# Performance work log

Hardware: AMD Instinct MI355X
Metric: run time of the kernel (lower is better)

## Reference

```python
import jax, jax.numpy as jnp
import numpy as np

NUM_HEADS = 16
NUM_KV_HEADS = 8
HEAD_DIM = 128
ROPE_THETA = 10000.0
SOFTCAP = 50.0


def rotate_half(x):
    x1, x2 = jnp.split(x, 2, axis=-1)
    return jnp.concatenate((-x2, x1), axis=-1)


def rope_cos_sin(seq_len):
    inv_freq = 1.0 / (ROPE_THETA ** (jnp.arange(0, HEAD_DIM, 2, dtype=jnp.float32) / HEAD_DIM))
    t = jnp.arange(seq_len, dtype=jnp.float32)
    freqs = t[:, None] * inv_freq[None, :]          # [S, D/2]
    emb = jnp.concatenate((freqs, freqs), axis=-1)  # [S, D]
    return jnp.cos(emb), jnp.sin(emb)


def setup_inputs() -> dict:
    key = jax.random.key(0)
    k1, k2, k3, k4, k5 = jax.random.split(key, 5)
    B, S, H = 2, 2048, 2048
    sc = 1.0 / np.sqrt(H)
    return {
        "hidden_states": jax.random.normal(k1, (B, S, H), dtype=jnp.float32),
        "Wq": jax.random.normal(k2, (H, NUM_HEADS * HEAD_DIM), dtype=jnp.float32) * sc,
        "Wk": jax.random.normal(k3, (H, NUM_KV_HEADS * HEAD_DIM), dtype=jnp.float32) * sc,
        "Wv": jax.random.normal(k4, (H, NUM_KV_HEADS * HEAD_DIM), dtype=jnp.float32) * sc,
        "Wo": jax.random.normal(k5, (NUM_HEADS * HEAD_DIM, H), dtype=jnp.float32) * sc,
    }


def reference(hidden_states, Wq, Wk, Wv, Wo):
    B, S, _ = hidden_states.shape
    groups = NUM_HEADS // NUM_KV_HEADS

    # projections -> [B, heads, S, D]
    q = (hidden_states @ Wq).reshape(B, S, NUM_HEADS, HEAD_DIM).transpose(0, 2, 1, 3)
    k = (hidden_states @ Wk).reshape(B, S, NUM_KV_HEADS, HEAD_DIM).transpose(0, 2, 1, 3)
    v = (hidden_states @ Wv).reshape(B, S, NUM_KV_HEADS, HEAD_DIM).transpose(0, 2, 1, 3)

    cos, sin = rope_cos_sin(S)  # [S, D], broadcast over (B, heads)
    q = q * cos + rotate_half(q) * sin
    k = k * cos + rotate_half(k) * sin

    # GQA: expand KV heads (repeat_interleave along head dim)
    k = jnp.repeat(k, groups, axis=1)
    v = jnp.repeat(v, groups, axis=1)

    scores = jnp.einsum('bhsd,bhtd->bhst', q, k) / np.sqrt(HEAD_DIM)
    scores = jnp.tanh(scores / SOFTCAP) * SOFTCAP  # Gemma logit softcapping
    weights = jax.nn.softmax(scores.astype(jnp.float32), axis=-1).astype(q.dtype)

    out = jnp.einsum('bhst,bhtd->bhsd', weights, v)
    out = out.transpose(0, 2, 1, 3).reshape(B, S, NUM_HEADS * HEAD_DIM)
    return out @ Wo
```

## Files before the change

kernel.cpp:

```cpp
#include <hip/hip_runtime.h>
#include <math.h>

typedef __bf16 bf16;
typedef __bf16 bf16x8 __attribute__((ext_vector_type(8)));
typedef __bf16 bf16x4 __attribute__((ext_vector_type(4)));
typedef float f32x2 __attribute__((ext_vector_type(2)));
typedef float f32x4 __attribute__((ext_vector_type(4)));
typedef float f32x16 __attribute__((ext_vector_type(16)));
typedef unsigned int uint;
typedef uint u32x4 __attribute__((ext_vector_type(4)));
typedef uint u32x2 __attribute__((ext_vector_type(2)));
typedef __bf16 bf16x8_a __attribute__((ext_vector_type(8), __may_alias__));
typedef uint u32x2_a __attribute__((ext_vector_type(2), __may_alias__));
typedef __bf16 bf16x4_a __attribute__((ext_vector_type(4), __may_alias__));
typedef __bf16 bf16_a __attribute__((__may_alias__));

constexpr int BATCH = 2;
constexpr int SEQ   = 2048;
constexpr int HID   = 2048;
constexpr int NHEAD = 16;
constexpr int NKV   = 8;
constexpr int HD    = 128;
constexpr int MROWS = BATCH * SEQ;

#define DEVINL __device__ __forceinline__

#define BAR()                                 \
  do {                                        \
    asm volatile("" ::: "memory");            \
    __builtin_amdgcn_s_barrier();             \
    asm volatile("" ::: "memory");            \
  } while (0)

#define WAITV(N) asm volatile("s_waitcnt vmcnt(" #N ")" ::: "memory")

DEVINL void async16(void* l, const void* g) {
  __builtin_amdgcn_global_load_lds((const __attribute__((address_space(1))) void*)g,
                                   (__attribute__((address_space(3))) void*)l, 16, 0, 0);
}

DEVINL f32x4 mfma16(bf16x8 a, bf16x8 b, f32x4 c) {
  return __builtin_amdgcn_mfma_f32_16x16x32_bf16(a, b, c, 0, 0, 0);
}
DEVINL f32x16 mfma32(bf16x8 a, bf16x8 b, f32x16 c) {
  return __builtin_amdgcn_mfma_f32_32x32x16_bf16(a, b, c, 0, 0, 0);
}

DEVINL f32x4 fzero4() { f32x4 z; z[0] = 0.f; z[1] = 0.f; z[2] = 0.f; z[3] = 0.f; return z; }

DEVINL float ex2(float x) {
#if __has_builtin(__builtin_amdgcn_exp2f)
  return __builtin_amdgcn_exp2f(x);
#else
  return __expf(x * 0.6931471805599453f);
#endif
}

DEVINL uint pkbf16(float lo, float hi) {
  unsigned short l = __builtin_bit_cast(unsigned short, (bf16)lo);
  unsigned short h = __builtin_bit_cast(unsigned short, (bf16)hi);
  return (uint)l | ((uint)h << 16);
}

DEVINL u32x2 pswap(uint a, uint b) {
#if __has_builtin(__builtin_amdgcn_permlane32_swap)
  return __builtin_amdgcn_permlane32_swap(a, b, false, false);
#else
  int hl = (int)((threadIdx.x >> 5) & 1);
  uint as = __shfl_xor(a, 32), bs = __shfl_xor(b, 32);
  u32x2 r;
  r[0] = hl ? bs : a;
  r[1] = hl ? b : as;
  return r;
#endif
}

__global__ __launch_bounds__(256) void prep(const float* __restrict__ X,
                                            const float* __restrict__ Wq,
                                            const float* __restrict__ Wk,
                                            const float* __restrict__ Wv,
                                            const float* __restrict__ Wo,
                                            bf16* __restrict__ Xb,
                                            bf16* __restrict__ WqT, bf16* __restrict__ WkT,
                                            bf16* __restrict__ WvT, bf16* __restrict__ WoT,
                                            float* __restrict__ ct, float* __restrict__ st) {
  const int tid = threadIdx.x;
  const int z = blockIdx.z;
  if (z == 4) {
    int idx = (blockIdx.y * 32 + blockIdx.x) * 256 + tid;
    if (idx < SEQ * 64) {
      int s = idx >> 6, d = idx & 63;
      float freq = powf(10000.0f, -(float)d * (1.0f / 64.0f));
      float a = (float)s * freq;
      ct[idx] = cosf(a);
      st[idx] = sinf(a);
    }
    return;
  }
  if (z == 5) {
    int j = (blockIdx.y * 32 + blockIdx.x) * 256 + tid;
#pragma unroll
    for (int it = 0; it < 8; it++) {
      int e = (it * 262144 + j) * 4;
      float4 v = *(const float4*)(X + e);
      bf16x4 o;
      o[0] = (bf16)v.x; o[1] = (bf16)v.y; o[2] = (bf16)v.z; o[3] = (bf16)v.w;
      *(bf16x4*)(Xb + e) = o;
    }
    return;
  }
  __shared__ bf16 t[64][65];
  const float* W; bf16* WT; int N;
  switch (z) {
    case 0: W = Wq; WT = WqT; N = 2048; break;
    case 1: W = Wk; WT = WkT; N = 1024; break;
    case 2: W = Wv; WT = WvT; N = 1024; break;
    default: W = Wo; WT = WoT; N = 2048; break;
  }
  int n0 = blockIdx.x * 64, k0 = blockIdx.y * 64;
  if (n0 >= N) return;
#pragma unroll
  for (int p = 0; p < 4; p++) {
    int r = (tid >> 4) + p * 16;
    int c4 = (tid & 15) * 4;
    float4 v = *(const float4*)(&W[(size_t)(k0 + r) * N + n0 + c4]);
    t[r][c4 + 0] = (bf16)v.x;
    t[r][c4 + 1] = (bf16)v.y;
    t[r][c4 + 2] = (bf16)v.z;
    t[r][c4 + 3] = (bf16)v.w;
  }
  __syncthreads();
#pragma unroll
  for (int p = 0; p < 4; p++) {
    int nr = (tid >> 4) + p * 16;
    int kb = (tid & 15) * 4;
    bf16x4 o;
    o[0] = t[kb + 0][nr];
    o[1] = t[kb + 1][nr];
    o[2] = t[kb + 2][nr];
    o[3] = t[kb + 3][nr];
    *(bf16x4_a*)(&WT[(size_t)(n0 + nr) * 2048 + k0 + kb]) = o;
  }
}

__global__ __launch_bounds__(256) void vtrans(const bf16* __restrict__ V, bf16* __restrict__ VT) {
  __shared__ bf16 t[64][65];
  int s0 = blockIdx.x * 64, d0 = blockIdx.y * 64;
  int bh = blockIdx.z, b = bh >> 3, kvh = bh & 7;
  for (int i = threadIdx.x; i < 4096; i += 256) {
    int r = i >> 6, c = i & 63;
    t[r][c] = V[(size_t)(b * SEQ + s0 + r) * (NKV * HD) + kvh * HD + d0 + c];
  }
  __syncthreads();
  for (int i = threadIdx.x; i < 4096; i += 256) {
    int r = i >> 6, c = i & 63;
    VT[((size_t)bh * HD + d0 + r) * SEQ + s0 + c] = t[c][r];
  }
}

template <int EPI>
__global__ __launch_bounds__(512, 2) void gemm8p(const bf16* __restrict__ A,
                                                 const bf16* __restrict__ BT,
                                                 void* __restrict__ C0, void* __restrict__ C1,
                                                 void* __restrict__ C2, int M, int N, int K,
                                                 const float* __restrict__ ct,
                                                 const float* __restrict__ st) {
  __shared__ alignas(16) char ldsA[65536];
  __shared__ alignas(16) char ldsB[65536];
  const int tid = threadIdx.x, lane = tid & 63, w = tid >> 6;
  const int l15 = lane & 15, l4 = lane >> 4;
  const int wm = w >> 2, wn = w & 3;
  const int gx = gridDim.x;
  const int nwg = gx * gridDim.y;
  int id = blockIdx.y * gx + blockIdx.x;
  id = (id & 7) * (nwg >> 3) + (id >> 3);
  const int row0 = (id / gx) * 256;
  const int col0 = (id % gx) * 256;

  f32x4 acc[8][4];
#pragma unroll
  for (int mt = 0; mt < 8; mt++)
#pragma unroll
    for (int nt = 0; nt < 4; nt++) acc[mt][nt] = fzero4();

  const int rG0 = tid >> 3, sG0 = ((tid & 7) ^ (rG0 & 7)) * 8;
  const int ci1 = 512 + tid;
  const int rG1 = ci1 >> 3, sG1 = ((ci1 & 7) ^ (rG1 & 7)) * 8;
  const int dst0 = tid * 16, dst1 = (512 + tid) * 16;

  const bf16* Asrc = A + (size_t)row0 * K;
  const bf16* Bsrc = BT + (size_t)col0 * K;
  const int nk = K >> 6;

#define STG_A(half, kt, buf)                                         \
  {                                                                  \
    char* d = ldsA + (buf) * 32768 + (half) * 16384;                 \
    const bf16* s = Asrc + (size_t)((half) * 128) * K + (kt) * 64;   \
    async16(d + dst0, s + (size_t)rG0 * K + sG0);                    \
    async16(d + dst1, s + (size_t)rG1 * K + sG1);                    \
  }
#define STG_B(half, kt, buf)                                         \
  {                                                                  \
    char* d = ldsB + (buf) * 32768 + (half) * 16384;                 \
    const bf16* s = Bsrc + (size_t)((half) * 128) * K + (kt) * 64;   \
    async16(d + dst0, s + (size_t)rG0 * K + sG0);                    \
    async16(d + dst1, s + (size_t)rG1 * K + sG1);                    \
  }

  STG_A(0, 0, 0) STG_A(1, 0, 0) STG_B(0, 0, 0) STG_B(1, 0, 0)
  STG_B(0, 1, 1) STG_B(1, 1, 1) STG_A(0, 1, 1) STG_A(1, 1, 1)
  WAITV(8);
  BAR();

  bf16x8 af[8];
  bf16x8 bfr[2][4];

  for (int t = 0; t < nk; ++t) {
    const int buf = t & 1;
    const char* bA = ldsA + buf * 32768 + wm * 16384;
    const char* bB = ldsB + buf * 32768;
    const bool s2 = (t + 2) < nk;

#pragma unroll
    for (int mtp = 0; mtp < 4; mtp++)
#pragma unroll
      for (int kc = 0; kc < 2; kc++) {
        int r = mtp * 16 + l15;
        int off = ((r << 7) + ((kc * 4 + l4) << 4)) ^ ((r & 7) << 4);
        af[mtp * 2 + kc] = *(const bf16x8_a*)(bA + off);
      }
#pragma unroll
    for (int ntp = 0; ntp < 2; ntp++)
#pragma unroll
      for (int kc = 0; kc < 2; kc++) {
        int c = wn * 16 + ntp * 64 + l15;
        int off = ((c << 7) + ((kc * 4 + l4) << 4)) ^ ((c & 7) << 4);
        bfr[0][ntp * 2 + kc] = *(const bf16x8_a*)(bB + off);
        bfr[1][ntp * 2 + kc] = *(const bf16x8_a*)(bB + 16384 + off);
      }
    BAR();
    if (s2) { STG_B(0, t + 2, buf) STG_B(1, t + 2, buf) }
    __builtin_amdgcn_s_setprio(1);
#pragma unroll
    for (int mtp = 0; mtp < 4; mtp++)
#pragma unroll
      for (int half = 0; half < 2; half++)
#pragma unroll
        for (int ntp = 0; ntp < 2; ntp++)
#pragma unroll
          for (int kc = 0; kc < 2; kc++)
            acc[mtp][half * 2 + ntp] =
                mfma16(af[mtp * 2 + kc], bfr[half][ntp * 2 + kc], acc[mtp][half * 2 + ntp]);
    __builtin_amdgcn_s_setprio(0);
    BAR();

#pragma unroll
    for (int mtp = 0; mtp < 4; mtp++)
#pragma unroll
      for (int kc = 0; kc < 2; kc++) {
        int r = 64 + mtp * 16 + l15;
        int off = ((r << 7) + ((kc * 4 + l4) << 4)) ^ ((r & 7) << 4);
        af[mtp * 2 + kc] = *(const bf16x8_a*)(bA + off);
      }
    BAR();
    if (s2) { STG_A(0, t + 2, buf) STG_A(1, t + 2, buf) }
    __builtin_amdgcn_s_setprio(1);
#pragma unroll
    for (int mtp = 0; mtp < 4; mtp++)
#pragma unroll
      for (int half = 0; half < 2; half++)
#pragma unroll
        for (int ntp = 0; ntp < 2; ntp++)
#pragma unroll
          for (int kc = 0; kc < 2; kc++)
            acc[mtp + 4][half * 2 + ntp] =
                mfma16(af[mtp * 2 + kc], bfr[half][ntp * 2 + kc], acc[mtp + 4][half * 2 + ntp]);
    __builtin_amdgcn_s_setprio(0);
    if (s2) { WAITV(8); } else { WAITV(0); }
    BAR();
  }
#undef STG_A
#undef STG_B

#pragma unroll
  for (int mt = 0; mt < 8; mt++)
#pragma unroll
    for (int nt = 0; nt < 4; nt++)
#pragma unroll
      for (int rg = 0; rg < 4; rg++) {
        int row = row0 + wm * 128 + mt * 16 + l4 * 4 + rg;
        int ntL = (nt & 1) + (nt >> 1) * 2;
        int cl = col0 + wn * 16 + ((nt >> 1) * 128) + ((nt & 1) * 64);
        (void)ntL;
        float v = acc[mt][nt][rg];
        cl += l15;
        if (EPI == 2) {
          ((float*)C0)[(size_t)row * N + cl] = v;
        } else {
          if (cl < 3072) {
            int s = row & (SEQ - 1);
            float cc = ct[s * 64 + wn * 16 + l15];
            float ss = st[s * 64 + wn * 16 + l15];
            float pv = acc[mt][nt ^ 1][rg];
            v = (nt & 1) ? fmaf(v, cc, pv * ss) : fmaf(v, cc, -pv * ss);
          }
          if (cl < 2048) {
            v *= 1.7677669529663689e-3f;
            ((bf16*)C0)[(size_t)row * 2048 + cl] = (bf16)v;
          } else if (cl < 3072) {
            ((bf16*)C1)[(size_t)row * 1024 + (cl - 2048)] = (bf16)v;
          } else {
            ((bf16*)C2)[(size_t)row * 1024 + (cl - 3072)] = (bf16)v;
          }
        }
      }
}

__global__ __launch_bounds__(512, 2) void gemm2p(const bf16* __restrict__ A,
                                                 const bf16* __restrict__ BT,
                                                 float* __restrict__ C, int M, int N, int K) {
  __shared__ alignas(16) char ldsA[65536];
  __shared__ alignas(16) char ldsB[49152];
  const int tid = threadIdx.x, lane = tid & 63, w = tid >> 6;
  const int l15 = lane & 15, l4 = lane >> 4;
  const int wm = w >> 1, wn = w & 1;
  const int gx = gridDim.x;
  const int nwg = gx * gridDim.y;
  int id = blockIdx.y * gx + blockIdx.x;
  id = (id & 7) * (nwg >> 3) + (id >> 3);
  const int row0 = (id / gx) * 256;
  const int col0 = (id % gx) * 128;

  f32x4 acc[4][4];
#pragma unroll
  for (int mt = 0; mt < 4; mt++)
#pragma unroll
    for (int nt = 0; nt < 4; nt++) acc[mt][nt] = fzero4();

  const int rG0 = tid >> 3, sG0 = ((tid & 7) ^ (rG0 & 7)) * 8;
  const int ci1 = 512 + tid;
  const int rG1 = ci1 >> 3, sG1 = ((ci1 & 7) ^ (rG1 & 7)) * 8;
  const int dst0 = tid * 16, dst1 = (512 + tid) * 16;

  const bf16* Asrc = A + (size_t)row0 * K;
  const bf16* Bsrc = BT + (size_t)col0 * K;
  const int nk = K >> 6;

#define STG_A2(half, kt, buf)                                        \
  {                                                                  \
    char* d = ldsA + (buf) * 32768 + (half) * 16384;                 \
    const bf16* s = Asrc + (size_t)((half) * 128) * K + (kt) * 64;   \
    async16(d + dst0, s + (size_t)rG0 * K + sG0);                    \
    async16(d + dst1, s + (size_t)rG1 * K + sG1);                    \
  }
#define STG_B2(kt, buf)                                              \
  {                                                                  \
    char* d = ldsB + (buf) * 16384;                                  \
    const bf16* s = Bsrc + (kt) * 64;                                \
    async16(d + dst0, s + (size_t)rG0 * K + sG0);                    \
    async16(d + dst1, s + (size_t)rG1 * K + sG1);                    \
  }

  STG_B2(0, 0) STG_A2(0, 0, 0) STG_A2(1, 0, 0)
  STG_B2(1, 1) STG_A2(0, 1, 1) STG_A2(1, 1, 1)
  WAITV(6);
  BAR();

  bf16x8 af[8];
  bf16x8 bfr[8];

  for (int t = 0; t < nk; ++t) {
    const int abuf = t & 1;
    int bb = t % 3;
    const char* bA = ldsA + abuf * 32768 + (wm >> 1) * 16384;
    const char* bB = ldsB + bb * 16384;
    const bool s2 = (t + 2) < nk;
    int bb2 = bb + 2; if (bb2 >= 3) bb2 -= 3;

#pragma unroll
    for (int mt = 0; mt < 4; mt++)
#pragma unroll
      for (int kc = 0; kc < 2; kc++) {
        int r = (wm & 1) * 64 + mt * 16 + l15;
        int off = ((r << 7) + ((kc * 4 + l4) << 4)) ^ ((r & 7) << 4);
        af[mt * 2 + kc] = *(const bf16x8_a*)(bA + off);
      }
#pragma unroll
    for (int nt = 0; nt < 4; nt++)
#pragma unroll
      for (int kc = 0; kc < 2; kc++) {
        int c = wn * 16 + nt * 32 + l15;
        int off = ((c << 7) + ((kc * 4 + l4) << 4)) ^ ((c & 7) << 4);
        bfr[nt * 2 + kc] = *(const bf16x8_a*)(bB + off);
      }
    BAR();
    if (s2) { STG_B2(t + 2, bb2) STG_A2(0, t + 2, abuf) STG_A2(1, t + 2, abuf) }
    __builtin_amdgcn_s_setprio(1);
#pragma unroll
    for (int mt = 0; mt < 4; mt++)
#pragma unroll
      for (int nt = 0; nt < 4; nt++)
#pragma unroll
        for (int kc = 0; kc < 2; kc++)
          acc[mt][nt] = mfma16(af[mt * 2 + kc], bfr[nt * 2 + kc], acc[mt][nt]);
    __builtin_amdgcn_s_setprio(0);
    if (s2) { WAITV(6); } else { WAITV(0); }
    BAR();
  }
#undef STG_A2
#undef STG_B2

#pragma unroll
  for (int mt = 0; mt < 4; mt++)
#pragma unroll
    for (int nt = 0; nt < 4; nt++)
#pragma unroll
      for (int rg = 0; rg < 4; rg++) {
        int row = row0 + wm * 64 + mt * 16 + l4 * 4 + rg;
        int cl = col0 + wn * 16 + nt * 32 + l15;
        C[(size_t)row * N + cl] = acc[mt][nt][rg];
      }
}

__global__ __launch_bounds__(512, 2) void attn10(const bf16* __restrict__ Q,
                                                 const bf16* __restrict__ Kg,
                                                 const bf16* __restrict__ VTg,
                                                 bf16* __restrict__ O) {
  __shared__ alignas(16) char ldsK[49152];
  __shared__ alignas(16) char ldsV[49152];
  const int tid = threadIdx.x, lane = tid & 63, w = tid >> 6;
  const int l31 = lane & 31, hl = lane >> 5;

  const int nx = gridDim.x, ny = gridDim.y;
  const int nwg = nx * ny * gridDim.z;
  int id = (blockIdx.z * ny + blockIdx.y) * nx + blockIdx.x;
  id = (id & 7) * (nwg >> 3) + (id >> 3);
  const int qt = id % nx; id /= nx;
  const int h = id % ny; const int b = id / ny;
  const int kvh = h >> 1;
  const int qrow = b * SEQ + qt * 256 + w * 32 + l31;

  bf16x8 qf[8];
  const bf16* qp = Q + (size_t)qrow * (NHEAD * HD) + h * HD + hl * 8;
#pragma unroll
  for (int kc = 0; kc < 8; kc++) qf[kc] = *(const bf16x8_a*)(qp + kc * 16);

  f32x16 oT[4];
#pragma unroll
  for (int dt = 0; dt < 4; dt++)
#pragma unroll
    for (int r = 0; r < 16; r++) oT[dt][r] = 0.f;
  f32x2 ls2; ls2[0] = 0.f; ls2[1] = 0.f;

  const int rK = tid >> 4, sK = (tid & 15) ^ (rK & 15);
  const int rV = tid >> 3, sV = (tid & 7) ^ (rV & 7);
  const size_t koff0 = (size_t)(b * SEQ + rK) * (NKV * HD) + kvh * HD + sK * 8;
  const size_t voff0 = ((size_t)(b * NKV + kvh) * HD + rV) * SEQ + sV * 8;

  const float Ac = 72.13475204444817f;
  const float Bc = -24.044917348149389f;

  auto STAGE = [&](int buf, int t) {
    char* dK = ldsK + buf * 16384;
    char* dV = ldsV + buf * 16384;
    const bf16* ks = Kg + koff0 + (size_t)t * (64 * NKV * HD);
    const bf16* vs = VTg + voff0 + (size_t)t * 64;
    async16(dK + tid * 16, ks);
    async16(dK + (512 + tid) * 16, ks + (size_t)32 * (NKV * HD));
    async16(dV + tid * 16, vs);
    async16(dV + (512 + tid) * 16, vs + (size_t)64 * SEQ);
  };

  const int kvr0 = l31, kvr1 = 32 + l31;

#define QKT(SC, lKp)                                                     \
  do {                                                                   \
    _Pragma("unroll")                                                    \
    for (int r = 0; r < 16; r++) { (SC)[0][r] = 0.f; (SC)[1][r] = 0.f; } \
    _Pragma("unroll")                                                    \
    for (int kc = 0; kc < 8; kc++) {                                     \
      int slot = kc * 2 + hl;                                            \
      int off0 = (kvr0 << 8) | ((slot ^ (kvr0 & 15)) << 4);              \
      int off1 = (kvr1 << 8) | ((slot ^ (kvr1 & 15)) << 4);              \
      bf16x8 kf0 = *(const bf16x8_a*)((lKp) + off0);                     \
      bf16x8 kf1 = *(const bf16x8_a*)((lKp) + off1);                     \
      (SC)[0] = mfma32(kf0, qf[kc], (SC)[0]);                            \
      (SC)[1] = mfma32(kf1, qf[kc], (SC)[1]);                            \
    }                                                                    \
  } while (0)

#define SOFTMAX(SC, PB)                                                  \
  do {                                                                   \
    _Pragma("unroll")                                                    \
    for (int ntb = 0; ntb < 2; ntb++) {                                  \
      uint u[4][2];                                                      \
      _Pragma("unroll")                                                  \
      for (int r2 = 0; r2 < 8; r2++) {                                   \
        f32x2 z; z[0] = (SC)[ntb][2 * r2]; z[1] = (SC)[ntb][2 * r2 + 1]; \
        f32x2 z2 = z * z;                                                \
        f32x2 wv = z2 * Bc + Ac;                                         \
        f32x2 e = z * wv;                                                \
        float p0 = ex2(e[0]), p1 = ex2(e[1]);                            \
        ls2[0] += p0; ls2[1] += p1;                                      \
        u[r2 >> 1][r2 & 1] = pkbf16(p0, p1);                             \
      }                                                                  \
      _Pragma("unroll")                                                  \
      for (int sub = 0; sub < 2; sub++) {                                \
        u32x2 r0 = pswap(u[2 * sub][0], u[2 * sub + 1][0]);              \
        u32x2 r1 = pswap(u[2 * sub][1], u[2 * sub + 1][1]);              \
        u32x4 bu;                                                        \
        bu[0] = r0[0];                                                   \
        bu[1] = r1[0];                                                   \
        bu[2] = r0[1];                                                   \
        bu[3] = r1[1];                                                   \
        (PB)[ntb * 2 + sub] = __builtin_bit_cast(bf16x8, bu);            \
      }                                                                  \
    }                                                                    \
  } while (0)

#define PVACC(PB, lVp)                                                   \
  do {                                                                   \
    _Pragma("unroll")                                                    \
    for (int kvb = 0; kvb < 4; kvb++) {                                  \
      int slot = kvb * 2 + hl;                                           \
      _Pragma("unroll")                                                  \
      for (int dt = 0; dt < 4; dt++) {                                   \
        int d = dt * 32 + l31;                                           \
        int off = (d << 7) | ((slot ^ (d & 7)) << 4);                    \
        bf16x8 vf = *(const bf16x8_a*)((lVp) + off);                     \
        oT[dt] = mfma32(vf, (PB)[kvb], oT[dt]);                          \
      }                                                                  \
    }                                                                    \
  } while (0)

  constexpr int NT = SEQ / 64;
  STAGE(0, 0);
  STAGE(1, 1);
  WAITV(4);
  BAR();

  f32x16 scA[2], scB[2];
  bf16x8 pb[4];
  QKT(scA, ldsK);

  for (int it = 0; it < NT / 2; ++it) {
    const int t0 = 2 * it;
    {
      const int t = t0;
      BAR();
      if (t + 2 < NT) STAGE((t + 2) % 3, t + 2);
      SOFTMAX(scA, pb);
      if (t + 2 < NT) { WAITV(4); } else { WAITV(0); }
      BAR();
      __builtin_amdgcn_s_setprio(1);
      if (t + 1 < NT) QKT(scB, ldsK + ((t + 1) % 3) * 16384);
      PVACC(pb, ldsV + (t % 3) * 16384);
      __builtin_amdgcn_s_setprio(0);
    }
    {
      const int t = t0 + 1;
      BAR();
      if (t + 2 < NT) STAGE((t + 2) % 3, t + 2);
      SOFTMAX(scB, pb);
      if (t + 2 < NT) { WAITV(4); } else { WAITV(0); }
      BAR();
      __builtin_amdgcn_s_setprio(1);
      if (t + 1 < NT) QKT(scA, ldsK + ((t + 1) % 3) * 16384);
      PVACC(pb, ldsV + (t % 3) * 16384);
      __builtin_amdgcn_s_setprio(0);
    }
  }
#undef QKT
#undef SOFTMAX
#undef PVACC

  float lsum = ls2[0] + ls2[1];
  float lsf = lsum + __shfl_xor(lsum, 32);
  float inv = 1.0f / lsf;
  bf16* ob = O + (size_t)qrow * (NHEAD * HD) + h * HD;
#pragma unroll
  for (int dt = 0; dt < 4; dt++)
#pragma unroll
    for (int g = 0; g < 4; g++) {
      u32x2 pr;
      pr[0] = pkbf16(oT[dt][4 * g] * inv, oT[dt][4 * g + 1] * inv);
      pr[1] = pkbf16(oT[dt][4 * g + 2] * inv, oT[dt][4 * g + 3] * inv);
      *(u32x2_a*)(ob + dt * 32 + 8 * g + 4 * hl) = pr;
    }
}

extern "C" void kernel_launch(void* const* d_in, const int* in_sizes, int n_in,
                              void* d_out, int out_size, void* d_ws, size_t ws_size,
                              hipStream_t stream) {
  const float* X  = (const float*)d_in[0];
  const float* Wq = (const float*)d_in[1];
  const float* Wk = (const float*)d_in[2];
  const float* Wv = (const float*)d_in[3];
  const float* Wo = (const float*)d_in[4];
  float* out = (float*)d_out;

  char* ws = (char*)d_ws;
  size_t off = 0;
  auto alloc = [&](size_t bytes) {
    void* p = ws + off;
    off += (bytes + 255) & ~(size_t)255;
    return p;
  };
  bf16* Xb  = (bf16*)alloc((size_t)MROWS * HID * 2);
  bf16* WqT = (bf16*)alloc((size_t)2048 * 2048 * 2);
  bf16* WkT = (bf16*)alloc((size_t)1024 * 2048 * 2);
  bf16* WvT = (bf16*)alloc((size_t)1024 * 2048 * 2);
  bf16* WoT = (bf16*)alloc((size_t)2048 * 2048 * 2);
  bf16* Qb  = (bf16*)alloc((size_t)MROWS * 2048 * 2);
  bf16* Kb  = (bf16*)alloc((size_t)MROWS * 1024 * 2);
  bf16* Vb  = (bf16*)alloc((size_t)MROWS * 1024 * 2);
  bf16* VTb = (bf16*)alloc((size_t)16 * 128 * 2048 * 2);
  bf16* AOb = (bf16*)alloc((size_t)MROWS * 2048 * 2);
  float* ct = (float*)alloc((size_t)SEQ * 64 * 4);
  float* st = (float*)alloc((size_t)SEQ * 64 * 4);

  prep<<<dim3(32, 32, 6), 256, 0, stream>>>(X, Wq, Wk, Wv, Wo, Xb, WqT, WkT, WvT, WoT, ct, st);
  gemm8p<1><<<dim3(16, 16), 512, 0, stream>>>(Xb, WqT, Qb, Kb, Vb, MROWS, 4096, 2048, ct, st);
  vtrans<<<dim3(32, 2, 16), 256, 0, stream>>>(Vb, VTb);
  attn10<<<dim3(8, 16, 2), 512, 0, stream>>>(Qb, Kb, VTb, AOb);
  gemm2p<<<dim3(16, 16), 512, 0, stream>>>(AOb, WoT, out, MROWS, 2048, 2048);

  (void)in_sizes; (void)n_in; (void)out_size; (void)ws_size;
}
```

Baseline: 235.6 us.

## Replace 256x256 pipelined QKV GEMM with simple 128x128 single-buffered kernel

Replaces the double-buffered 256x256-tile, 512-thread QKV projection GEMM with a 128x128-tile, 256-thread kernel. It loads each K-step into LDS with a full wait and barrier, with no prefetch overlap. The RoPE epilogue is rewritten to pair columns nt and nt+4 within one 128-column tile. This gives more, smaller workgroups and less LDS per block, at the cost of losing load/compute overlap and cutting data reuse per tile.

```diff
diff --git a/kernel.cpp b/kernel.cpp
--- a/kernel.cpp
+++ b/kernel.cpp
@@ -158,160 +158,92 @@
   }
 }
 
-template <int EPI>
-__global__ __launch_bounds__(512, 2) void gemm8p(const bf16* __restrict__ A,
-                                                 const bf16* __restrict__ BT,
-                                                 void* __restrict__ C0, void* __restrict__ C1,
-                                                 void* __restrict__ C2, int M, int N, int K,
-                                                 const float* __restrict__ ct,
-                                                 const float* __restrict__ st) {
-  __shared__ alignas(16) char ldsA[65536];
-  __shared__ alignas(16) char ldsB[65536];
+__global__ __launch_bounds__(256) void gemmA(const bf16* __restrict__ A,
+                                             const bf16* __restrict__ BT,
+                                             bf16* __restrict__ C0, bf16* __restrict__ C1,
+                                             bf16* __restrict__ C2, int K,
+                                             const float* __restrict__ ct,
+                                             const float* __restrict__ st) {
+  __shared__ alignas(16) char ldsA[16384];
+  __shared__ alignas(16) char ldsB[16384];
   const int tid = threadIdx.x, lane = tid & 63, w = tid >> 6;
   const int l15 = lane & 15, l4 = lane >> 4;
-  const int wm = w >> 2, wn = w & 3;
-  const int gx = gridDim.x;
+  const int gx = 32;
   const int nwg = gx * gridDim.y;
   int id = blockIdx.y * gx + blockIdx.x;
   id = (id & 7) * (nwg >> 3) + (id >> 3);
-  const int row0 = (id / gx) * 256;
-  const int col0 = (id % gx) * 256;
-
-  f32x4 acc[8][4];
-#pragma unroll
-  for (int mt = 0; mt < 8; mt++)
-#pragma unroll
-    for (int nt = 0; nt < 4; nt++) acc[mt][nt] = fzero4();
-
-  const int rG0 = tid >> 3, sG0 = ((tid & 7) ^ (rG0 & 7)) * 8;
-  const int ci1 = 512 + tid;
-  const int rG1 = ci1 >> 3, sG1 = ((ci1 & 7) ^ (rG1 & 7)) * 8;
-  const int dst0 = tid * 16, dst1 = (512 + tid) * 16;
+  const int row0 = (id / gx) * 128;
+  const int col0 = (id % gx) * 128;
+
+  f32x4 acc[2][8];
+#pragma unroll
+  for (int mt = 0; mt < 2; mt++)
+#pragma unroll
+    for (int nt = 0; nt < 8; nt++) acc[mt][nt] = fzero4();
 
   const bf16* Asrc = A + (size_t)row0 * K;
   const bf16* Bsrc = BT + (size_t)col0 * K;
   const int nk = K >> 6;
 
-#define STG_A(half, kt, buf)                                         \
-  {                                                                  \
-    char* d = ldsA + (buf) * 32768 + (half) * 16384;                 \
-    const bf16* s = Asrc + (size_t)((half) * 128) * K + (kt) * 64;   \
-    async16(d + dst0, s + (size_t)rG0 * K + sG0);                    \
-    async16(d + dst1, s + (size_t)rG1 * K + sG1);                    \
-  }
-#define STG_B(half, kt, buf)                                         \
-  {                                                                  \
-    char* d = ldsB + (buf) * 32768 + (half) * 16384;                 \
-    const bf16* s = Bsrc + (size_t)((half) * 128) * K + (kt) * 64;   \
-    async16(d + dst0, s + (size_t)rG0 * K + sG0);                    \
-    async16(d + dst1, s + (size_t)rG1 * K + sG1);                    \
-  }
-
-  STG_A(0, 0, 0) STG_A(1, 0, 0) STG_B(0, 0, 0) STG_B(1, 0, 0)
-  STG_B(0, 1, 1) STG_B(1, 1, 1) STG_A(0, 1, 1) STG_A(1, 1, 1)
-  WAITV(8);
-  BAR();
-
-  bf16x8 af[8];
-  bf16x8 bfr[2][4];
-
   for (int t = 0; t < nk; ++t) {
-    const int buf = t & 1;
-    const char* bA = ldsA + buf * 32768 + wm * 16384;
-    const char* bB = ldsB + buf * 32768;
-    const bool s2 = (t + 2) < nk;
-
-#pragma unroll
-    for (int mtp = 0; mtp < 4; mtp++)
+    const int k0 = t << 6;
+    BAR();
+#pragma unroll
+    for (int j = 0; j < 4; j++) {
+      int ci = j * 256 + tid;
+      int r = ci >> 3, ps = ci & 7, ls = ps ^ (r & 7);
+      async16(ldsA + ci * 16, Asrc + (size_t)r * K + k0 + ls * 8);
+      async16(ldsB + ci * 16, Bsrc + (size_t)r * K + k0 + ls * 8);
+    }
+    WAITV(0);
+    BAR();
+
+    bf16x8 af[2][2];
+#pragma unroll
+    for (int mt = 0; mt < 2; mt++)
 #pragma unroll
       for (int kc = 0; kc < 2; kc++) {
-        int r = mtp * 16 + l15;
+        int r = w * 32 + mt * 16 + l15;
         int off = ((r << 7) + ((kc * 4 + l4) << 4)) ^ ((r & 7) << 4);
-        af[mtp * 2 + kc] = *(const bf16x8_a*)(bA + off);
+        af[mt][kc] = *(const bf16x8_a*)(ldsA + off);
       }
 #pragma unroll
-    for (int ntp = 0; ntp < 2; ntp++)
+    for (int nt = 0; nt < 8; nt++) {
 #pragma unroll
       for (int kc = 0; kc < 2; kc++) {
-        int c = wn * 16 + ntp * 64 + l15;
+        int c = nt * 16 + l15;
         int off = ((c << 7) + ((kc * 4 + l4) << 4)) ^ ((c & 7) << 4);
-        bfr[0][ntp * 2 + kc] = *(const bf16x8_a*)(bB + off);
-        bfr[1][ntp * 2 + kc] = *(const bf16x8_a*)(bB + 16384 + off);
+        bf16x8 bfr = *(const bf16x8_a*)(ldsB + off);
+        acc[0][nt] = mfma16(af[0][kc], bfr, acc[0][nt]);
+        acc[1][nt] = mfma16(af[1][kc], bfr, acc[1][nt]);
       }
-    BAR();
-    if (s2) { STG_B(0, t + 2, buf) STG_B(1, t + 2, buf) }
-    __builtin_amdgcn_s_setprio(1);
-#pragma unroll
-    for (int mtp = 0; mtp < 4; mtp++)
-#pragma unroll
-      for (int half = 0; half < 2; half++)
-#pragma unroll
-        for (int ntp = 0; ntp < 2; ntp++)
-#pragma unroll
-          for (int kc = 0; kc < 2; kc++)
-            acc[mtp][half * 2 + ntp] =
-                mfma16(af[mtp * 2 + kc], bfr[half][ntp * 2 + kc], acc[mtp][half * 2 + ntp]);
-    __builtin_amdgcn_s_setprio(0);
-    BAR();
-
-#pragma unroll
-    for (int mtp = 0; mtp < 4; mtp++)
-#pragma unroll
-      for (int kc = 0; kc < 2; kc++) {
-        int r = 64 + mtp * 16 + l15;
-        int off = ((r << 7) + ((kc * 4 + l4) << 4)) ^ ((r & 7) << 4);
-        af[mtp * 2 + kc] = *(const bf16x8_a*)(bA + off);
-      }
-    BAR();
-    if (s2) { STG_A(0, t + 2, buf) STG_A(1, t + 2, buf) }
-    __builtin_amdgcn_s_setprio(1);
-#pragma unroll
-    for (int mtp = 0; mtp < 4; mtp++)
-#pragma unroll
-      for (int half = 0; half < 2; half++)
-#pragma unroll
-        for (int ntp = 0; ntp < 2; ntp++)
-#pragma unroll
-          for (int kc = 0; kc < 2; kc++)
-            acc[mtp + 4][half * 2 + ntp] =
-                mfma16(af[mtp * 2 + kc], bfr[half][ntp * 2 + kc], acc[mtp + 4][half * 2 + ntp]);
-    __builtin_amdgcn_s_setprio(0);
-    if (s2) { WAITV(8); } else { WAITV(0); }
-    BAR();
-  }
-#undef STG_A
-#undef STG_B
-
-#pragma unroll
-  for (int mt = 0; mt < 8; mt++)
-#pragma unroll
-    for (int nt = 0; nt < 4; nt++)
+    }
+  }
+
+#pragma unroll
+  for (int mt = 0; mt < 2; mt++)
+#pragma unroll
+    for (int nt = 0; nt < 8; nt++)
 #pragma unroll
       for (int rg = 0; rg < 4; rg++) {
-        int row = row0 + wm * 128 + mt * 16 + l4 * 4 + rg;
-        int ntL = (nt & 1) + (nt >> 1) * 2;
-        int cl = col0 + wn * 16 + ((nt >> 1) * 128) + ((nt & 1) * 64);
-        (void)ntL;
+        int row = row0 + w * 32 + mt * 16 + l4 * 4 + rg;
+        int cl = col0 + nt * 16 + l15;
         float v = acc[mt][nt][rg];
-        cl += l15;
-        if (EPI == 2) {
-          ((float*)C0)[(size_t)row * N + cl] = v;
+        if (cl < 3072) {
+          int s = row & (SEQ - 1);
+          int ntp = (nt < 4) ? nt + 4 : nt - 4;
+          float pv = (nt < 4) ? -acc[mt][ntp][rg] : acc[mt][ntp][rg];
+          float cc = ct[s * 64 + (cl & 63)];
+          float ss = st[s * 64 + (cl & 63)];
+          v = fmaf(v, cc, pv * ss);
+        }
+        if (cl < 2048) {
+          v *= 1.7677669529663689e-3f;
+          C0[(size_t)row * 2048 + cl] = (bf16)v;
+        } else if (cl < 3072) {
+          C1[(size_t)row * 1024 + (cl - 2048)] = (bf16)v;
         } else {
-          if (cl < 3072) {
-            int s = row & (SEQ - 1);
-            float cc = ct[s * 64 + wn * 16 + l15];
-            float ss = st[s * 64 + wn * 16 + l15];
-            float pv = acc[mt][nt ^ 1][rg];
-            v = (nt & 1) ? fmaf(v, cc, pv * ss) : fmaf(v, cc, -pv * ss);
-          }
-          if (cl < 2048) {
-            v *= 1.7677669529663689e-3f;
-            ((bf16*)C0)[(size_t)row * 2048 + cl] = (bf16)v;
-          } else if (cl < 3072) {
-            ((bf16*)C1)[(size_t)row * 1024 + (cl - 2048)] = (bf16)v;
-          } else {
-            ((bf16*)C2)[(size_t)row * 1024 + (cl - 3072)] = (bf16)v;
-          }
+          C2[(size_t)row * 1024 + (cl - 3072)] = (bf16)v;
         }
       }
 }
@@ -620,7 +552,7 @@
   float* st = (float*)alloc((size_t)SEQ * 64 * 4);
 
   prep<<<dim3(32, 32, 6), 256, 0, stream>>>(X, Wq, Wk, Wv, Wo, Xb, WqT, WkT, WvT, WoT, ct, st);
-  gemm8p<1><<<dim3(16, 16), 512, 0, stream>>>(Xb, WqT, Qb, Kb, Vb, MROWS, 4096, 2048, ct, st);
+  gemmA<<<dim3(32, 32), 256, 0, stream>>>(Xb, WqT, Qb, Kb, Vb, 2048, ct, st);
   vtrans<<<dim3(32, 2, 16), 256, 0, stream>>>(Vb, VTb);
   attn10<<<dim3(8, 16, 2), 512, 0, stream>>>(Qb, Kb, VTb, AOb);
   gemm2p<<<dim3(16, 16), 512, 0, stream>>>(AOb, WoT, out, MROWS, 2048, 2048);
```

Result: slower. 263.6 us (+11.9%).
